# Performance work log

Hardware: AMD Instinct MI355X
Metric: run time of the kernel (lower is better)

## Reference

```python
import jax, jax.numpy as jnp
import numpy as np

N, F_IN, F_OUT = 8192, 256, 128
ALPHA = 0.2  # LeakyReLU negative slope
NEG_BIG = -9e15


def setup_inputs() -> dict:
    key = jax.random.key(0)
    k1, k2, k3, k4 = jax.random.split(key, 4)
    h = jax.random.normal(k1, (N, F_IN), dtype=jnp.float32)
    adj = jax.random.randint(k2, (N, N), 0, 2, dtype=jnp.int32)
    # Xavier-uniform-ish scaled params (gain 1.414)
    w_bound = 1.414 * np.sqrt(6.0 / (F_IN + F_OUT))
    a_bound = 1.414 * np.sqrt(6.0 / (2 * F_OUT + 1))
    W = jax.random.uniform(k3, (F_IN, F_OUT), jnp.float32, -w_bound, w_bound)
    a = jax.random.uniform(k4, (2 * F_OUT, 1), jnp.float32, -a_bound, a_bound)
    return {"h": h, "adj": adj, "W": W, "a": a}


def reference(h, adj, W, a):
    # Wh: [N, F_OUT]
    Wh = h @ W
    # a = [a1; a2]; e_ij = leakyrelu(a1.Wh_i + a2.Wh_j) == the torch concat+matmul,
    # computed via broadcast-add instead of materializing [N, N, 2F].
    a1 = a[:F_OUT, 0]   # [F_OUT]
    a2 = a[F_OUT:, 0]   # [F_OUT]
    si = Wh @ a1        # [N]
    sj = Wh @ a2        # [N]
    e = jax.nn.leaky_relu(si[:, None] + sj[None, :], negative_slope=ALPHA)  # [N, N]
    logits = jnp.where(adj > 0, e, NEG_BIG)
    attention = jax.nn.softmax(logits, axis=1)
    # dropout is identity in eval mode (training=False)
    h_prime = attention @ Wh  # [N, F_OUT]
    return jax.nn.elu(h_prime)  # concat=True path
```

## Files before the change

kernel.cpp:

```cpp
#include <hip/hip_runtime.h>

#define NN 8192
#define FIN 256
#define FOUT 128
#define BKJ 64
#define JSPLIT 8
#define LALPHA 0.2f

typedef short bf16x8 __attribute__((ext_vector_type(8)));
typedef float f32x4 __attribute__((ext_vector_type(4)));

#define FOR8(X) X(0) X(1) X(2) X(3) X(4) X(5) X(6) X(7)
#define FOR4(X) X(0) X(1) X(2) X(3)

static __device__ __forceinline__ unsigned short f2bf(float f) {
    unsigned u = __float_as_uint(f);
    u += 0x7FFFu + ((u >> 16) & 1u);
    return (unsigned short)(u >> 16);
}

__global__ __launch_bounds__(256) void gat_k1(
    const float* __restrict__ h, const float* __restrict__ W,
    const float* __restrict__ a, unsigned short* __restrict__ WhT,
    float* __restrict__ si, float* __restrict__ sj)
{
    __shared__ float Wt[64 * 128];
    __shared__ float hT[64 * 36 + 4];
    const int t = threadIdx.x;
    const int r0 = blockIdx.x * 32;
    const int rg = t >> 5;
    const int cg = t & 31;
    float acc[4][4] = {{0.f,0.f,0.f,0.f},{0.f,0.f,0.f,0.f},{0.f,0.f,0.f,0.f},{0.f,0.f,0.f,0.f}};

    for (int kc = 0; kc < 4; ++kc) {
        __syncthreads();
        const float4* Ws = (const float4*)(W + kc * 64 * FOUT);
        float4* Wd = (float4*)Wt;
        #pragma unroll
        for (int v = 0; v < 8; ++v) Wd[v * 256 + t] = Ws[v * 256 + t];
        {
            const int hr = t >> 3, hk = (t & 7) * 8;
            const float* hs = h + (size_t)(r0 + hr) * FIN + kc * 64 + hk;
            float4 x0 = *(const float4*)hs;
            float4 x1 = *(const float4*)(hs + 4);
            hT[(hk + 0) * 36 + hr] = x0.x; hT[(hk + 1) * 36 + hr] = x0.y;
            hT[(hk + 2) * 36 + hr] = x0.z; hT[(hk + 3) * 36 + hr] = x0.w;
            hT[(hk + 4) * 36 + hr] = x1.x; hT[(hk + 5) * 36 + hr] = x1.y;
            hT[(hk + 6) * 36 + hr] = x1.z; hT[(hk + 7) * 36 + hr] = x1.w;
        }
        __syncthreads();
        #pragma unroll 8
        for (int kk = 0; kk < 64; ++kk) {
            float4 hv4 = *(const float4*)&hT[kk * 36 + rg * 4];
            float4 wv4 = *(const float4*)&Wt[kk * 128 + cg * 4];
            float hv[4] = {hv4.x, hv4.y, hv4.z, hv4.w};
            float wv[4] = {wv4.x, wv4.y, wv4.z, wv4.w};
            #pragma unroll
            for (int rr = 0; rr < 4; ++rr)
                #pragma unroll
                for (int cc = 0; cc < 4; ++cc)
                    acc[rr][cc] = fmaf(hv[rr], wv[cc], acc[rr][cc]);
        }
    }
    float4 a1v4 = *(const float4*)(a + cg * 4);
    float4 a2v4 = *(const float4*)(a + FOUT + cg * 4);
    float a1v[4] = {a1v4.x, a1v4.y, a1v4.z, a1v4.w};
    float a2v[4] = {a2v4.x, a2v4.y, a2v4.z, a2v4.w};
    float ps[4], qs[4];
    #pragma unroll
    for (int rr = 0; rr < 4; ++rr) {
        float p = 0.f, q = 0.f;
        #pragma unroll
        for (int cc = 0; cc < 4; ++cc) {
            p = fmaf(acc[rr][cc], a1v[cc], p);
            q = fmaf(acc[rr][cc], a2v[cc], q);
        }
        ps[rr] = p; qs[rr] = q;
    }
    #pragma unroll
    for (int off = 1; off <= 16; off <<= 1) {
        #pragma unroll
        for (int rr = 0; rr < 4; ++rr) {
            ps[rr] += __shfl_xor(ps[rr], off);
            qs[rr] += __shfl_xor(qs[rr], off);
        }
    }
    if (cg == 0) {
        #pragma unroll
        for (int rr = 0; rr < 4; ++rr) {
            si[r0 + rg * 4 + rr] = ps[rr];
            sj[r0 + rg * 4 + rr] = qs[rr];
        }
    }
    #pragma unroll
    for (int cc = 0; cc < 4; ++cc) {
        ushort4 v;
        v.x = f2bf(acc[0][cc]); v.y = f2bf(acc[1][cc]);
        v.z = f2bf(acc[2][cc]); v.w = f2bf(acc[3][cc]);
        *(ushort4*)(WhT + (size_t)(cg * 4 + cc) * NN + r0 + rg * 4) = v;
    }
}

__global__ __launch_bounds__(256) void gat_k1s(
    const float* __restrict__ sj, float* __restrict__ sjmax)
{
    __shared__ float red[256];
    float m = -1e30f;
    for (int i = threadIdx.x; i < NN; i += 256) m = fmaxf(m, sj[i]);
    red[threadIdx.x] = m;
    __syncthreads();
    for (int o = 128; o > 0; o >>= 1) {
        if (threadIdx.x < o) red[threadIdx.x] = fmaxf(red[threadIdx.x], red[threadIdx.x + o]);
        __syncthreads();
    }
    if (threadIdx.x == 0) sjmax[0] = red[0];
}

static __device__ __forceinline__ unsigned short pcalc(
    int a, float sjv, float si_l, float m_row)
{
    float x = si_l + sjv;
    x = fmaxf(x, LALPHA * x);
    float p = (a > 0) ? __expf(x - m_row) : 0.f;
    return f2bf(p);
}

template<int JS, bool FINAL>
__global__ __launch_bounds__(256, 4) void gat_k2(
    const int* __restrict__ adj, const unsigned short* __restrict__ WhT,
    const float* __restrict__ si, const float* __restrict__ sj,
    const float* __restrict__ sjmaxp,
    float* __restrict__ lsum, float* __restrict__ Opart, float* __restrict__ out)
{
    const int JR_ = NN / JS;
    const int NST_ = JR_ / BKJ;
    __shared__ __align__(16) unsigned short tile[2][8192];
    const int t = threadIdx.x;
    const int w = t >> 6, l = t & 63;
    const int rb = (int)blockIdx.x / JS, js = (int)blockIdx.x % JS;
    const int iw = rb * 64 + w * 16;
    const int j0 = js * JR_;
    const int row = l & 15, kg = l >> 4;

    const float si_l = si[iw + row];
    const float sjmax = sjmaxp[0];
    const float xm = si_l + sjmax;
    const float m_row = fmaxf(xm, LALPHA * xm);
    const float* sjb = sj + j0 + kg * 8;
    const int* adjb = adj + (size_t)(iw + row) * NN + j0 + kg * 8;

#define GSRC_D(v) const unsigned short* gsrc##v = WhT + (size_t)(v * 32 + (t >> 3)) * NN + j0 + (t & 7) * 8; \
                  const int ldo##v = ((v * 256 + t) * 16) ^ (((t >> 3) & 7) << 4);
    FOR4(GSRC_D)

#define REG_D(v) int4 stg##v, adr##v;
    FOR4(REG_D)
#define STG_L0(v) stg##v = *(const int4*)(gsrc##v);
    FOR4(STG_L0)
#define ADR_L0(q) adr##q = *(const int4*)(adjb + (q / 2) * 32 + (q % 2) * 4);
    FOR4(ADR_L0)

#define ACC_D(n) f32x4 acc##n = {0.f, 0.f, 0.f, 0.f};
    FOR8(ACC_D)
    f32x4 acc8 = {0.f, 0.f, 0.f, 0.f};
    bf16x8 ones;
    #pragma unroll
    for (int z = 0; z < 8; ++z) ones[z] = (short)0x3F80;
    const int kg16 = kg * 16;

#define STG_WR(v) *(int4*)((char*)tb + ldo##v) = stg##v;
#define STG_LN(v) stg##v = *(const int4*)(gsrc##v + so);
#define ADR_LN(q) adr##q = *(const int4*)(adjb + so + (q / 2) * 32 + (q % 2) * 4);
#define P8(AF, A0, A1, sp) { \
    float4 s0_ = *(const float4*)(sp); float4 s1_ = *(const float4*)((sp) + 4); \
    AF[0] = (short)pcalc(A0.x, s0_.x, si_l, m_row); \
    AF[1] = (short)pcalc(A0.y, s0_.y, si_l, m_row); \
    AF[2] = (short)pcalc(A0.z, s0_.z, si_l, m_row); \
    AF[3] = (short)pcalc(A0.w, s0_.w, si_l, m_row); \
    AF[4] = (short)pcalc(A1.x, s1_.x, si_l, m_row); \
    AF[5] = (short)pcalc(A1.y, s1_.y, si_l, m_row); \
    AF[6] = (short)pcalc(A1.z, s1_.z, si_l, m_row); \
    AF[7] = (short)pcalc(A1.w, s1_.w, si_l, m_row); }
#define MFMA_ROW(n) { const int c_ = n * 16 + row; \
    const int off_ = c_ * 128 + ((KB ^ ((c_ & 7) << 4))); \
    bf16x8 bv_ = *(const bf16x8*)((const char*)tb + off_); \
    acc##n = __builtin_amdgcn_mfma_f32_16x16x32_bf16(AFk, bv_, acc##n, 0, 0, 0); }
#define MFMA_KC(afv, kcl) { const bf16x8 AFk = afv; const int KB = kcl * 64 + kg16; FOR8(MFMA_ROW) \
    acc8 = __builtin_amdgcn_mfma_f32_16x16x32_bf16(AFk, ones, acc8, 0, 0, 0); }

    for (int s = 0; s < NST_; ++s) {
        unsigned short* tb = tile[s & 1];
        FOR4(STG_WR)
        if (s + 1 < NST_) {
            const size_t so = (size_t)(s + 1) * BKJ;
            FOR4(STG_LN)
        }
        bf16x8 af0, af1;
        {
            const float* spp = sjb + s * BKJ;
            P8(af0, adr0, adr1, spp)
            P8(af1, adr2, adr3, spp + 32)
        }
        if (s + 1 < NST_) {
            const size_t so = (size_t)(s + 1) * BKJ;
            FOR4(ADR_LN)
        }
        __syncthreads();
        MFMA_KC(af0, 0) MFMA_KC(af1, 1)
    }

    if (FINAL) {
#define FN_ROW(n) { size_t ob = (size_t)(iw + kg * 4) * FOUT + n * 16 + row; \
    float o0 = acc##n[0] / acc8[0]; out[ob]            = (o0 > 0.f) ? o0 : expm1f(o0); \
    float o1 = acc##n[1] / acc8[1]; out[ob + FOUT]     = (o1 > 0.f) ? o1 : expm1f(o1); \
    float o2 = acc##n[2] / acc8[2]; out[ob + 2 * FOUT] = (o2 > 0.f) ? o2 : expm1f(o2); \
    float o3 = acc##n[3] / acc8[3]; out[ob + 3 * FOUT] = (o3 > 0.f) ? o3 : expm1f(o3); }
        FOR8(FN_ROW)
    } else {
        if (row == 0) {
            #pragma unroll
            for (int q = 0; q < 4; ++q)
                lsum[(size_t)js * NN + iw + kg * 4 + q] = acc8[q];
        }
#define ST_ROW(n) { size_t ob = ((size_t)js * NN + iw + kg * 4) * FOUT + n * 16 + row; \
    Opart[ob] = acc##n[0]; Opart[ob + FOUT] = acc##n[1]; \
    Opart[ob + 2 * FOUT] = acc##n[2]; Opart[ob + 3 * FOUT] = acc##n[3]; }
        FOR8(ST_ROW)
    }
}

__global__ __launch_bounds__(256) void gat_k3(
    const float* __restrict__ lsum, const float* __restrict__ Opart,
    float* __restrict__ out)
{
    const int t = threadIdx.x;
    const int i = (int)blockIdx.x * 2 + (t >> 7);
    const int f = t & 127;
    float den = 0.f, num = 0.f;
    const size_t SP = (size_t)NN * FOUT;
    size_t base = (size_t)i * FOUT + f;
    #pragma unroll
    for (int k = 0; k < JSPLIT; ++k) {
        den += lsum[(size_t)k * NN + i];
        num += Opart[(size_t)k * SP + base];
    }
    float o = num / den;
    out[base] = (o > 0.f) ? o : expm1f(o);
}

extern "C" void kernel_launch(void* const* d_in, const int* in_sizes, int n_in,
                              void* d_out, int out_size, void* d_ws, size_t ws_size,
                              hipStream_t stream) {
    const float* h  = (const float*)d_in[0];
    const int*  adj = (const int*)d_in[1];
    const float* W  = (const float*)d_in[2];
    const float* a  = (const float*)d_in[3];
    float* out = (float*)d_out;
    char* ws = (char*)d_ws;
    unsigned short* WhT = (unsigned short*)ws;
    float* si     = (float*)(ws + 2097152);
    float* sj     = (float*)(ws + 2129920);
    float* sjmax  = (float*)(ws + 2162688);
    float* lsum   = (float*)(ws + 2162944);
    float* Opart  = (float*)(ws + 2425088);
    const size_t need = 2425088 + (size_t)JSPLIT * NN * FOUT * 4;

    gat_k1<<<256, 256, 0, stream>>>(h, W, a, WhT, si, sj);
    gat_k1s<<<1, 256, 0, stream>>>(sj, sjmax);
    if (ws_size >= need) {
        gat_k2<JSPLIT, false><<<128 * JSPLIT, 256, 0, stream>>>(adj, WhT, si, sj, sjmax, lsum, Opart, out);
        gat_k3<<<4096, 256, 0, stream>>>(lsum, Opart, out);
    } else {
        gat_k2<1, true><<<128, 256, 0, stream>>>(adj, WhT, si, sj, sjmax, lsum, Opart, out);
    }
}
```

Baseline: 111.1 us.

## Double K-tile depth, halve J-split, use exp2 with prescaled logits and packed bf16 convert

Raises the per-stage j tile from 64 to 128 and cuts the j-split from 8 to 4. This gives fewer, larger stages and a smaller partial buffer to reduce, in exchange for twice the LDS and a lower occupancy bound. The softmax exponent moves to base-2: sj is prescaled by log2e in the first kernel and per-row constants are hoisted, so each element needs two adds, a max, a select and a v_exp_f32, with hardware packed bf16 conversion. The loop is reordered to compute probabilities before the staging writes, with explicit waitcnt, barrier and sched barriers.

Measured after the change: 98.02 us. -11.8%, faster.

```diff
diff --git a/kernel.cpp b/kernel.cpp
--- a/kernel.cpp
+++ b/kernel.cpp
@@ -3,26 +3,33 @@
 #define NN 8192
 #define FIN 256
 #define FOUT 128
-#define BKJ 64
-#define JSPLIT 8
+#define BKJ 128
+#define JSPLIT 4
 #define LALPHA 0.2f
+#define NEGB -9.0e15f
+#define LOG2E 1.4426950408889634f
 
 typedef short bf16x8 __attribute__((ext_vector_type(8)));
 typedef float f32x4 __attribute__((ext_vector_type(4)));
 
 #define FOR8(X) X(0) X(1) X(2) X(3) X(4) X(5) X(6) X(7)
-#define FOR4(X) X(0) X(1) X(2) X(3)
 
 static __device__ __forceinline__ unsigned short f2bf(float f) {
     unsigned u = __float_as_uint(f);
     u += 0x7FFFu + ((u >> 16) & 1u);
     return (unsigned short)(u >> 16);
 }
+static __device__ __forceinline__ float ex2(float x) {
+    float r; asm("v_exp_f32 %0, %1" : "=v"(r) : "v"(x)); return r;
+}
+static __device__ __forceinline__ int cvtpk(float lo, float hi) {
+    int r; asm("v_cvt_pk_bf16_f32 %0, %1, %2" : "=v"(r) : "v"(lo), "v"(hi)); return r;
+}
 
 __global__ __launch_bounds__(256) void gat_k1(
     const float* __restrict__ h, const float* __restrict__ W,
     const float* __restrict__ a, unsigned short* __restrict__ WhT,
-    float* __restrict__ si, float* __restrict__ sj)
+    float* __restrict__ si, float* __restrict__ sj, float* __restrict__ sjl)
 {
     __shared__ float Wt[64 * 128];
     __shared__ float hT[64 * 36 + 4];
@@ -90,6 +97,7 @@
         for (int rr = 0; rr < 4; ++rr) {
             si[r0 + rg * 4 + rr] = ps[rr];
             sj[r0 + rg * 4 + rr] = qs[rr];
+            sjl[r0 + rg * 4 + rr] = qs[rr] * LOG2E;
         }
     }
     #pragma unroll
@@ -116,25 +124,24 @@
     if (threadIdx.x == 0) sjmax[0] = red[0];
 }
 
-static __device__ __forceinline__ unsigned short pcalc(
-    int a, float sjv, float si_l, float m_row)
-{
-    float x = si_l + sjv;
-    x = fmaxf(x, LALPHA * x);
-    float p = (a > 0) ? __expf(x - m_row) : 0.f;
-    return f2bf(p);
+static __device__ __forceinline__ float pe(int av, float sjlv, float a2, float b2) {
+    float t1 = a2 + sjlv;
+    float t2 = fmaf(0.2f, sjlv, b2);
+    float y = fmaxf(t1, t2);
+    y = (av > 0) ? y : NEGB;
+    return ex2(y);
 }
 
 template<int JS, bool FINAL>
-__global__ __launch_bounds__(256, 4) void gat_k2(
+__global__ __launch_bounds__(256, 2) void gat_k2(
     const int* __restrict__ adj, const unsigned short* __restrict__ WhT,
-    const float* __restrict__ si, const float* __restrict__ sj,
+    const float* __restrict__ si, const float* __restrict__ sjl,
     const float* __restrict__ sjmaxp,
     float* __restrict__ lsum, float* __restrict__ Opart, float* __restrict__ out)
 {
     const int JR_ = NN / JS;
     const int NST_ = JR_ / BKJ;
-    __shared__ __align__(16) unsigned short tile[2][8192];
+    __shared__ __align__(16) unsigned short tile[2][16384];
     const int t = threadIdx.x;
     const int w = t >> 6, l = t & 63;
     const int rb = (int)blockIdx.x / JS, js = (int)blockIdx.x % JS;
@@ -146,19 +153,21 @@
     const float sjmax = sjmaxp[0];
     const float xm = si_l + sjmax;
     const float m_row = fmaxf(xm, LALPHA * xm);
-    const float* sjb = sj + j0 + kg * 8;
+    const float a2 = (si_l - m_row) * LOG2E;
+    const float b2 = (LALPHA * si_l - m_row) * LOG2E;
+    const float* sjb = sjl + j0 + kg * 8;
     const int* adjb = adj + (size_t)(iw + row) * NN + j0 + kg * 8;
 
-#define GSRC_D(v) const unsigned short* gsrc##v = WhT + (size_t)(v * 32 + (t >> 3)) * NN + j0 + (t & 7) * 8; \
-                  const int ldo##v = ((v * 256 + t) * 16) ^ (((t >> 3) & 7) << 4);
-    FOR4(GSRC_D)
+#define GSRC_D(v) const unsigned short* gsrc##v = WhT + (size_t)(v * 16 + (t >> 4)) * NN + j0 + (t & 15) * 8; \
+                  const int ldo##v = ((v * 256 + t) * 16) ^ (((t >> 4) & 7) << 4);
+    FOR8(GSRC_D)
 
 #define REG_D(v) int4 stg##v, adr##v;
-    FOR4(REG_D)
+    FOR8(REG_D)
 #define STG_L0(v) stg##v = *(const int4*)(gsrc##v);
-    FOR4(STG_L0)
+    FOR8(STG_L0)
 #define ADR_L0(q) adr##q = *(const int4*)(adjb + (q / 2) * 32 + (q % 2) * 4);
-    FOR4(ADR_L0)
+    FOR8(ADR_L0)
 
 #define ACC_D(n) f32x4 acc##n = {0.f, 0.f, 0.f, 0.f};
     FOR8(ACC_D)
@@ -173,16 +182,15 @@
 #define ADR_LN(q) adr##q = *(const int4*)(adjb + so + (q / 2) * 32 + (q % 2) * 4);
 #define P8(AF, A0, A1, sp) { \
     float4 s0_ = *(const float4*)(sp); float4 s1_ = *(const float4*)((sp) + 4); \
-    AF[0] = (short)pcalc(A0.x, s0_.x, si_l, m_row); \
-    AF[1] = (short)pcalc(A0.y, s0_.y, si_l, m_row); \
-    AF[2] = (short)pcalc(A0.z, s0_.z, si_l, m_row); \
-    AF[3] = (short)pcalc(A0.w, s0_.w, si_l, m_row); \
-    AF[4] = (short)pcalc(A1.x, s1_.x, si_l, m_row); \
-    AF[5] = (short)pcalc(A1.y, s1_.y, si_l, m_row); \
-    AF[6] = (short)pcalc(A1.z, s1_.z, si_l, m_row); \
-    AF[7] = (short)pcalc(A1.w, s1_.w, si_l, m_row); }
+    float p0_ = pe(A0.x, s0_.x, a2, b2), p1_ = pe(A0.y, s0_.y, a2, b2); \
+    float p2_ = pe(A0.z, s0_.z, a2, b2), p3_ = pe(A0.w, s0_.w, a2, b2); \
+    float p4_ = pe(A1.x, s1_.x, a2, b2), p5_ = pe(A1.y, s1_.y, a2, b2); \
+    float p6_ = pe(A1.z, s1_.z, a2, b2), p7_ = pe(A1.w, s1_.w, a2, b2); \
+    int4 w_; w_.x = cvtpk(p0_, p1_); w_.y = cvtpk(p2_, p3_); \
+    w_.z = cvtpk(p4_, p5_); w_.w = cvtpk(p6_, p7_); \
+    AF = __builtin_bit_cast(bf16x8, w_); }
 #define MFMA_ROW(n) { const int c_ = n * 16 + row; \
-    const int off_ = c_ * 128 + ((KB ^ ((c_ & 7) << 4))); \
+    const int off_ = c_ * 256 + ((KB ^ ((c_ & 7) << 4))); \
     bf16x8 bv_ = *(const bf16x8*)((const char*)tb + off_); \
     acc##n = __builtin_amdgcn_mfma_f32_16x16x32_bf16(AFk, bv_, acc##n, 0, 0, 0); }
 #define MFMA_KC(afv, kcl) { const bf16x8 AFk = afv; const int KB = kcl * 64 + kg16; FOR8(MFMA_ROW) \
@@ -190,23 +198,28 @@
 
     for (int s = 0; s < NST_; ++s) {
         unsigned short* tb = tile[s & 1];
-        FOR4(STG_WR)
-        if (s + 1 < NST_) {
-            const size_t so = (size_t)(s + 1) * BKJ;
-            FOR4(STG_LN)
-        }
-        bf16x8 af0, af1;
+        bf16x8 af0, af1, af2, af3;
         {
             const float* spp = sjb + s * BKJ;
             P8(af0, adr0, adr1, spp)
             P8(af1, adr2, adr3, spp + 32)
+            P8(af2, adr4, adr5, spp + 64)
+            P8(af3, adr6, adr7, spp + 96)
         }
         if (s + 1 < NST_) {
             const size_t so = (size_t)(s + 1) * BKJ;
-            FOR4(ADR_LN)
-        }
-        __syncthreads();
-        MFMA_KC(af0, 0) MFMA_KC(af1, 1)
+            FOR8(ADR_LN)
+        }
+        FOR8(STG_WR)
+        if (s + 1 < NST_) {
+            const size_t so = (size_t)(s + 1) * BKJ;
+            FOR8(STG_LN)
+        }
+        __builtin_amdgcn_sched_barrier(0);
+        asm volatile("s_waitcnt lgkmcnt(0)" ::: "memory");
+        __builtin_amdgcn_s_barrier();
+        __builtin_amdgcn_sched_barrier(0);
+        MFMA_KC(af0, 0) MFMA_KC(af1, 1) MFMA_KC(af2, 2) MFMA_KC(af3, 3)
     }
 
     if (FINAL) {
@@ -260,17 +273,18 @@
     unsigned short* WhT = (unsigned short*)ws;
     float* si     = (float*)(ws + 2097152);
     float* sj     = (float*)(ws + 2129920);
-    float* sjmax  = (float*)(ws + 2162688);
-    float* lsum   = (float*)(ws + 2162944);
-    float* Opart  = (float*)(ws + 2425088);
-    const size_t need = 2425088 + (size_t)JSPLIT * NN * FOUT * 4;
-
-    gat_k1<<<256, 256, 0, stream>>>(h, W, a, WhT, si, sj);
+    float* sjl    = (float*)(ws + 2162688);
+    float* sjmax  = (float*)(ws + 2195456);
+    float* lsum   = (float*)(ws + 2195712);
+    float* Opart  = (float*)(ws + 2326784);
+    const size_t need = 2326784 + (size_t)JSPLIT * NN * FOUT * 4;
+
+    gat_k1<<<256, 256, 0, stream>>>(h, W, a, WhT, si, sj, sjl);
     gat_k1s<<<1, 256, 0, stream>>>(sj, sjmax);
     if (ws_size >= need) {
-        gat_k2<JSPLIT, false><<<128 * JSPLIT, 256, 0, stream>>>(adj, WhT, si, sj, sjmax, lsum, Opart, out);
+        gat_k2<JSPLIT, false><<<128 * JSPLIT, 256, 0, stream>>>(adj, WhT, si, sjl, sjmax, lsum, Opart, out);
         gat_k3<<<4096, 256, 0, stream>>>(lsum, Opart, out);
     } else {
-        gat_k2<1, true><<<128, 256, 0, stream>>>(adj, WhT, si, sj, sjmax, lsum, Opart, out);
-    }
-}
+        gat_k2<1, true><<<128, 256, 0, stream>>>(adj, WhT, si, sjl, sjmax, lsum, Opart, out);
+    }
+}
```
